# Performance work log

Hardware: AMD Instinct MI355X
Metric: run time of the kernel (lower is better)

Reference implementation:

```python
import jax, jax.numpy as jnp
import numpy as np

N = 50000        # nodes
E = 800000       # edges
IN, H1, H2 = 512, 256, 128
NEG_SLOPE = 0.2


def setup_inputs() -> dict:
    key = jax.random.key(0)
    k = jax.random.split(key, 6)
    X = jax.random.normal(k[0], (N, IN), jnp.float32)
    edge_index = jax.random.randint(k[1], (2, E), 0, N, dtype=jnp.int64)
    # GCNConv params: linear weight (no bias in lin) + additive bias
    W1 = jax.random.normal(k[2], (IN, H1), jnp.float32) / np.sqrt(IN).astype(np.float32)
    b1 = jnp.zeros((H1,), jnp.float32)
    W2 = jax.random.normal(k[3], (H1, H2), jnp.float32) / np.sqrt(H1).astype(np.float32)
    b2 = jnp.zeros((H2,), jnp.float32)
    return {"X": X, "edge_index": edge_index, "W1": W1, "b1": b1, "W2": W2, "b2": b2}


def gcn_conv(x, edge_index, W, b):
    """PyG GCNConv: X' = D^{-1/2} (A + I) D^{-1/2} (X W) + b."""
    src, dst = edge_index[0], edge_index[1]
    # degree with self-loops (unit edge weights)
    deg = jnp.zeros((N,), x.dtype).at[dst].add(jnp.asarray(1.0, x.dtype)) + 1.0
    dinv = jax.lax.rsqrt(deg)
    h = x @ W                                   # dense transform first (in >= out)
    coef = dinv[src] * dinv[dst]                # [E]
    msgs = h[src] * coef[:, None]               # [E, out]
    agg = jax.ops.segment_sum(msgs, dst, num_segments=N)
    agg = agg + (dinv * dinv)[:, None] * h      # self-loop contribution
    return agg + b


def reference(X, edge_index, W1, b1, W2, b2):
    Z = jax.nn.leaky_relu(gcn_conv(X, edge_index, W1, b1), NEG_SLOPE)
    Z = jax.nn.leaky_relu(gcn_conv(Z, edge_index, W2, b2), NEG_SLOPE)
    return Z
```

## Files before the change

### kernel.cpp

```cpp
#include <hip/hip_runtime.h>

constexpr int N_NODES = 50000;
constexpr int N_EDGES = 800000;
constexpr int F_IN  = 512;
constexpr int F_H1  = 256;
constexpr int F_H2  = 128;

typedef short  short8  __attribute__((ext_vector_type(8)));
typedef float  f32x4   __attribute__((ext_vector_type(4)));
typedef unsigned short us4 __attribute__((ext_vector_type(4)));

__device__ __forceinline__ unsigned short bf16_rn(float f) {
  unsigned int u = __float_as_uint(f);
  return (unsigned short)((u + 0x7FFFu + ((u >> 16) & 1u)) >> 16);
}
__device__ __forceinline__ float bf16_tof(unsigned short h) {
  return __uint_as_float(((unsigned int)h) << 16);
}


__global__ __launch_bounds__(256) void k_count(const int* __restrict__ dst,
                                               int* __restrict__ cnt, int e) {
  int i = blockIdx.x * 256 + threadIdx.x;
  if (i < e) atomicAdd(&cnt[dst[i]], 1);
}

__global__ __launch_bounds__(1024) void k_scan(const int* __restrict__ cnt,
                                               int* __restrict__ rowstart,
                                               int* __restrict__ cursor,
                                               float* __restrict__ dinv, int n) {
  __shared__ int wsum[16];
  __shared__ int carry_s;
  const int t = threadIdx.x;
  const int wid = t >> 6, lane = t & 63;
  if (t == 0) { carry_s = 0; rowstart[0] = 0; }
  __syncthreads();
  for (int base = 0; base < n; base += 4096) {
    const int i0 = base + t * 4;
    int v[4];
    if (i0 + 4 <= n) {
      const int4 v4 = *(const int4*)&cnt[i0];
      v[0] = v4.x; v[1] = v4.y; v[2] = v4.z; v[3] = v4.w;
    } else {
#pragma unroll
      for (int j = 0; j < 4; ++j) v[j] = (i0 + j < n) ? cnt[i0 + j] : 0;
    }
#pragma unroll
    for (int j = 0; j < 4; ++j)
      if (i0 + j < n) dinv[i0 + j] = rsqrtf((float)v[j] + 1.0f);
    const int tsum = v[0] + v[1] + v[2] + v[3];
    int x = tsum;
#pragma unroll
    for (int off = 1; off < 64; off <<= 1) {
      int y = __shfl_up(x, off);
      if (lane >= off) x += y;
    }
    if (lane == 63) wsum[wid] = x;
    __syncthreads();
    if (wid == 0) {
      int s = (lane < 16) ? wsum[lane] : 0;
#pragma unroll
      for (int off = 1; off < 16; off <<= 1) {
        int y = __shfl_up(s, off);
        if (lane >= off) s += y;
      }
      if (lane < 16) wsum[lane] = s;
    }
    __syncthreads();
    const int carry = carry_s;
    const int woff = (wid == 0) ? 0 : wsum[wid - 1];
    int run = carry + woff + x - tsum;
#pragma unroll
    for (int j = 0; j < 4; ++j) {
      if (i0 + j < n) {
        cursor[i0 + j] = run;
        run += v[j];
        rowstart[i0 + j + 1] = run;
      }
    }
    __syncthreads();
    if (t == 1023) carry_s = carry + woff + x;
    __syncthreads();
  }
}

__global__ __launch_bounds__(256) void k_fill(const int* __restrict__ src,
                                              const int* __restrict__ dst,
                                              int* __restrict__ cursor,
                                              const float* __restrict__ dinv,
                                              int2* __restrict__ csr, int e) {
  int i = blockIdx.x * 256 + threadIdx.x;
  if (i < e) {
    const int s = src[i], d = dst[i];
    int slot = atomicAdd(&cursor[d], 1);
    csr[slot] = make_int2(s, __float_as_int(dinv[s] * dinv[d]));
  }
}

__global__ __launch_bounds__(256) void k_wsplit2(const float* __restrict__ W1,
                                                 unsigned short* __restrict__ W1h,
                                                 unsigned short* __restrict__ W1l,
                                                 const float* __restrict__ W2,
                                                 unsigned short* __restrict__ W2h,
                                                 unsigned short* __restrict__ W2l) {
  constexpr int T1 = F_IN * F_H1;
  constexpr int T2 = F_H1 * F_H2;
  int id = blockIdx.x * 256 + threadIdx.x;
  if (id < T1) {
    int n = id / F_IN, k = id - n * F_IN;
    float f = W1[(size_t)k * F_H1 + n];
    unsigned short h = bf16_rn(f);
    W1h[id] = h;
    W1l[id] = bf16_rn(f - bf16_tof(h));
  } else if (id < T1 + T2) {
    int id2 = id - T1;
    int n = id2 / F_H1, k = id2 - n * F_H1;
    float f = W2[(size_t)k * F_H2 + n];
    unsigned short h = bf16_rn(f);
    W2h[id2] = h;
    W2l[id2] = bf16_rn(f - bf16_tof(h));
  }
}

template <bool A_IS_F32>
__global__ __launch_bounds__(256) void k_mm(const float* __restrict__ Af,
                                            const unsigned short* __restrict__ Ah,
                                            const unsigned short* __restrict__ Al,
                                            const unsigned short* __restrict__ Bth,
                                            const unsigned short* __restrict__ Btl,
                                            float* __restrict__ C,
                                            unsigned short* __restrict__ Cb,
                                            int M, int N, int K) {
  __shared__ unsigned short Ah_s[128 * 64];
  __shared__ unsigned short Al_s[128 * 64];
  __shared__ unsigned short Bh_s[128 * 64];
  __shared__ unsigned short Bl_s[128 * 64];
  const int tid = threadIdx.x;
  const int wid = tid >> 6, lane = tid & 63;
  const int wm = wid >> 1, wn = wid & 1;
  const int lr = lane & 15, lg = lane >> 4;
  const int row0 = blockIdx.x * 128, col0 = blockIdx.y * 128;

  f32x4 acc[4][4] = {};

  float4 af0[4], af1[4];
  short8 ahr[4], alr[4];
  short8 bhr[4], blr[4];

  const int r_ld = tid >> 3, g_ld = tid & 7;
  const bool arow_ok = (row0 + r_ld) < M;

  auto load_tile = [&](int k0) {
#pragma unroll
    for (int c = 0; c < 4; ++c) {
      const int r = c * 32 + r_ld;
      const int gr = row0 + r;
      if (A_IS_F32) {
        af0[c] = make_float4(0.f, 0.f, 0.f, 0.f);
        af1[c] = af0[c];
        if (gr < M) {
          const float* ap = Af + (size_t)gr * K + k0 + g_ld * 8;
          af0[c] = *(const float4*)ap;
          af1[c] = *(const float4*)(ap + 4);
        }
      } else {
        ahr[c] = short8{};
        alr[c] = short8{};
        if (gr < M) {
          ahr[c] = *(const short8*)&Ah[(size_t)gr * K + k0 + g_ld * 8];
          alr[c] = *(const short8*)&Al[(size_t)gr * K + k0 + g_ld * 8];
        }
      }
      const int gcol = col0 + r;
      bhr[c] = *(const short8*)&Bth[(size_t)gcol * K + k0 + g_ld * 8];
      blr[c] = *(const short8*)&Btl[(size_t)gcol * K + k0 + g_ld * 8];
    }
  };

  auto store_tile = [&]() {
#pragma unroll
    for (int c = 0; c < 4; ++c) {
      const int r = c * 32 + r_ld;
      const int gs = g_ld ^ (r & 7);
      const int doff = r * 64 + gs * 8;
      if (A_IS_F32) {
        const float fv[8] = {af0[c].x, af0[c].y, af0[c].z, af0[c].w,
                             af1[c].x, af1[c].y, af1[c].z, af1[c].w};
        unsigned short hv[8], lv[8];
#pragma unroll
        for (int j = 0; j < 8; ++j) {
          hv[j] = bf16_rn(fv[j]);
          lv[j] = bf16_rn(fv[j] - bf16_tof(hv[j]));
        }
        us4* dh = (us4*)&Ah_s[doff];
        us4* dl = (us4*)&Al_s[doff];
        dh[0] = us4{hv[0], hv[1], hv[2], hv[3]};
        dh[1] = us4{hv[4], hv[5], hv[6], hv[7]};
        dl[0] = us4{lv[0], lv[1], lv[2], lv[3]};
        dl[1] = us4{lv[4], lv[5], lv[6], lv[7]};
      } else {
        *(short8*)&Ah_s[doff] = ahr[c];
        *(short8*)&Al_s[doff] = alr[c];
      }
      *(short8*)&Bh_s[doff] = bhr[c];
      *(short8*)&Bl_s[doff] = blr[c];
    }
  };

  const int nsteps = K >> 6;
  load_tile(0);
  for (int s = 0; s < nsteps; ++s) {
    store_tile();
    __syncthreads();
    if (s + 1 < nsteps) load_tile((s + 1) << 6);
#pragma unroll
    for (int kk = 0; kk < 2; ++kk) {
      short8 ah[4], al[4], bh[4], bl[4];
#pragma unroll
      for (int m = 0; m < 4; ++m) {
        const int r = wm * 64 + m * 16 + lr;
        const int g = kk * 4 + lg;
        const int off = r * 64 + (g ^ (r & 7)) * 8;
        ah[m] = *(const short8*)&Ah_s[off];
        al[m] = *(const short8*)&Al_s[off];
      }
#pragma unroll
      for (int n = 0; n < 4; ++n) {
        const int r = wn * 64 + n * 16 + lr;
        const int g = kk * 4 + lg;
        const int off = r * 64 + (g ^ (r & 7)) * 8;
        bh[n] = *(const short8*)&Bh_s[off];
        bl[n] = *(const short8*)&Bl_s[off];
      }
#pragma unroll
      for (int m = 0; m < 4; ++m)
#pragma unroll
        for (int n = 0; n < 4; ++n)
          acc[m][n] = __builtin_amdgcn_mfma_f32_16x16x32_bf16(ah[m], bh[n],
                                                              acc[m][n], 0, 0, 0);
#pragma unroll
      for (int m = 0; m < 4; ++m)
#pragma unroll
        for (int n = 0; n < 4; ++n) {
          acc[m][n] = __builtin_amdgcn_mfma_f32_16x16x32_bf16(ah[m], bl[n],
                                                              acc[m][n], 0, 0, 0);
          acc[m][n] = __builtin_amdgcn_mfma_f32_16x16x32_bf16(al[m], bh[n],
                                                              acc[m][n], 0, 0, 0);
        }
    }
    __syncthreads();
  }
#pragma unroll
  for (int m = 0; m < 4; ++m) {
#pragma unroll
    for (int j = 0; j < 4; ++j) {
      const int row = row0 + wm * 64 + m * 16 + (lane >> 4) * 4 + j;
      if (row < M) {
        const size_t boff = (size_t)row * N + col0 + wn * 64 + (lane & 15);
        float* cp = C + boff;
#pragma unroll
        for (int n = 0; n < 4; ++n) cp[n * 16] = acc[m][n][j];
        if (Cb) {
          unsigned short* cbp = Cb + boff;
#pragma unroll
          for (int n = 0; n < 4; ++n) cbp[n * 16] = bf16_rn(acc[m][n][j]);
        }
      }
    }
  }
}

template <int F, bool SPLIT_OUT, bool BF16G>
__global__ __launch_bounds__(256) void k_agg(const float* __restrict__ hf,
                                             const unsigned short* __restrict__ hb,
                                             const int* __restrict__ rowstart,
                                             const int2* __restrict__ csr,
                                             const float* __restrict__ dinv,
                                             const float* __restrict__ bias,
                                             float* __restrict__ outp,
                                             unsigned short* __restrict__ outh,
                                             unsigned short* __restrict__ outl,
                                             int n) {
  constexpr int V = F / 64;
  const int node = (blockIdx.x * 256 + threadIdx.x) >> 6;
  const int lane = threadIdx.x & 63;
  if (node >= n) return;
  const float dn = dinv[node];
  const int e0 = rowstart[node];
  const int cnt = rowstart[node + 1] - e0;
  const int2* cp = csr + e0;
  float acc[V] = {};
  int i = 0;

  auto gather = [&](int s, float f[V]) {
    if constexpr (BF16G) {
      if constexpr (V == 4) {
        const uint2 u = *(const uint2*)(hb + (size_t)s * F + lane * 4);
        f[0] = __uint_as_float(u.x << 16);
        f[1] = __uint_as_float(u.x & 0xffff0000u);
        f[2] = __uint_as_float(u.y << 16);
        f[3] = __uint_as_float(u.y & 0xffff0000u);
      } else {
        const unsigned int u = *(const unsigned int*)(hb + (size_t)s * F + lane * 2);
        f[0] = __uint_as_float(u << 16);
        f[1] = __uint_as_float(u & 0xffff0000u);
      }
    } else {
      if constexpr (V == 4) {
        const float4 v = *(const float4*)(hf + (size_t)s * F + lane * 4);
        f[0] = v.x; f[1] = v.y; f[2] = v.z; f[3] = v.w;
      } else {
        const float2 v = *(const float2*)(hf + (size_t)s * F + lane * 2);
        f[0] = v.x; f[1] = v.y;
      }
    }
  };

  for (; i + 4 <= cnt; i += 4) {
    const int2 p0 = cp[i], p1 = cp[i + 1], p2 = cp[i + 2], p3 = cp[i + 3];
    float f0[V], f1[V], f2[V], f3[V];
    gather(p0.x, f0);
    gather(p1.x, f1);
    gather(p2.x, f2);
    gather(p3.x, f3);
    const float c0 = __int_as_float(p0.y), c1 = __int_as_float(p1.y);
    const float c2 = __int_as_float(p2.y), c3 = __int_as_float(p3.y);
#pragma unroll
    for (int j = 0; j < V; ++j)
      acc[j] += c0 * f0[j] + c1 * f1[j] + c2 * f2[j] + c3 * f3[j];
  }
  for (; i < cnt; ++i) {
    const int2 p = cp[i];
    const float c = __int_as_float(p.y);
    float f[V];
    gather(p.x, f);
#pragma unroll
    for (int j = 0; j < V; ++j) acc[j] += c * f[j];
  }

  const float sc = dn * dn;
  const float* hp = hf + (size_t)node * F + lane * V;
  const float* bp = bias + lane * V;
  float r[V];
#pragma unroll
  for (int j = 0; j < V; ++j) {
    float t = acc[j] + sc * hp[j] + bp[j];
    r[j] = fmaxf(t, 0.2f * t);
  }
  if constexpr (SPLIT_OUT) {
    unsigned short hh[V], ll[V];
#pragma unroll
    for (int j = 0; j < V; ++j) {
      hh[j] = bf16_rn(r[j]);
      ll[j] = bf16_rn(r[j] - bf16_tof(hh[j]));
    }
    if constexpr (V == 4) {
      *(us4*)&outh[(size_t)node * F + lane * 4] = us4{hh[0], hh[1], hh[2], hh[3]};
      *(us4*)&outl[(size_t)node * F + lane * 4] = us4{ll[0], ll[1], ll[2], ll[3]};
    } else {
#pragma unroll
      for (int j = 0; j < V; ++j) {
        outh[(size_t)node * F + lane * V + j] = hh[j];
        outl[(size_t)node * F + lane * V + j] = ll[j];
      }
    }
  } else {
    float* op = outp + (size_t)node * F + lane * V;
    if constexpr (V == 4) {
      *(float4*)op = make_float4(r[0], r[1], r[2], r[3]);
    } else {
      *(float2*)op = make_float2(r[0], r[1]);
    }
  }
}

extern "C" void kernel_launch(void* const* d_in, const int* in_sizes, int n_in,
                              void* d_out, int out_size, void* d_ws, size_t ws_size,
                              hipStream_t stream) {
  const float* X  = (const float*)d_in[0];
  const int*   ei = (const int*)d_in[1];
  const float* W1 = (const float*)d_in[2];
  const float* b1 = (const float*)d_in[3];
  const float* W2 = (const float*)d_in[4];
  const float* b2 = (const float*)d_in[5];
  float* out = (float*)d_out;
  const int* src = ei;
  const int* dst = ei + N_EDGES;

  char* p0 = (char*)d_ws;
  char* p = p0;
  float* h1 = (float*)p;                    p += (size_t)N_NODES * F_H1 * 4;
  unsigned short* z1h = (unsigned short*)p; p += (size_t)N_NODES * F_H1 * 2;
  unsigned short* z1l = (unsigned short*)p; p += (size_t)N_NODES * F_H1 * 2;
  unsigned short* Wt1h = (unsigned short*)p; p += (size_t)F_IN * F_H1 * 2;
  unsigned short* Wt1l = (unsigned short*)p; p += (size_t)F_IN * F_H1 * 2;
  unsigned short* Wt2h = (unsigned short*)p; p += (size_t)F_H1 * F_H2 * 2;
  unsigned short* Wt2l = (unsigned short*)p; p += (size_t)F_H1 * F_H2 * 2;
  float* dinv = (float*)p;                  p += 50048 * 4;
  int* counts = (int*)p;                    p += 50048 * 4;
  int* rowstart = (int*)p;                  p += 50056 * 4;
  int* cursor = (int*)p;                    p += 50048 * 4;
  int2* csr = (int2*)p;                     p += (size_t)N_EDGES * 8;
  unsigned short* h1b = (unsigned short*)p; p += (size_t)N_NODES * F_H1 * 2;
  unsigned short* h2b = h1b;
  float* h2 = h1;
  const bool GB = (size_t)(p - p0) <= ws_size;

  hipMemsetAsync(counts, 0, N_NODES * sizeof(int), stream);
  k_count<<<(N_EDGES + 255) / 256, 256, 0, stream>>>(dst, counts, N_EDGES);
  k_scan<<<1, 1024, 0, stream>>>(counts, rowstart, cursor, dinv, N_NODES);
  k_fill<<<(N_EDGES + 255) / 256, 256, 0, stream>>>(src, dst, cursor, dinv, csr,
                                                    N_EDGES);

  k_wsplit2<<<(F_IN * F_H1 + F_H1 * F_H2 + 255) / 256, 256, 0, stream>>>(
      W1, Wt1h, Wt1l, W2, Wt2h, Wt2l);

  dim3 g1((N_NODES + 127) / 128, F_H1 / 128);
  k_mm<true><<<g1, 256, 0, stream>>>(X, nullptr, nullptr, Wt1h, Wt1l, h1,
                                     GB ? h1b : nullptr, N_NODES, F_H1, F_IN);
  if (GB)
    k_agg<F_H1, true, true><<<(N_NODES + 3) / 4, 256, 0, stream>>>(
        h1, h1b, rowstart, csr, dinv, b1, nullptr, z1h, z1l, N_NODES);
  else
    k_agg<F_H1, true, false><<<(N_NODES + 3) / 4, 256, 0, stream>>>(
        h1, nullptr, rowstart, csr, dinv, b1, nullptr, z1h, z1l, N_NODES);

  dim3 g2((N_NODES + 127) / 128, F_H2 / 128);
  k_mm<false><<<g2, 256, 0, stream>>>(nullptr, z1h, z1l, Wt2h, Wt2l, h2,
                                      GB ? h2b : nullptr, N_NODES, F_H2, F_H1);
  if (GB)
    k_agg<F_H2, false, true><<<(N_NODES + 3) / 4, 256, 0, stream>>>(
        h2, h2b, rowstart, csr, dinv, b2, out, nullptr, nullptr, N_NODES);
  else
    k_agg<F_H2, false, false><<<(N_NODES + 3) / 4, 256, 0, stream>>>(
        h2, nullptr, rowstart, csr, dinv, b2, out, nullptr, nullptr, N_NODES);
}
```

Baseline: 348.8 us.

## Store GEMM output as bf16 hi/lo pairs and use 8-wave GEMM blocks

The GEMM now writes its result as a bf16 high/low split instead of fp32 plus an optional bf16 copy. Aggregation gathers only the high half and rebuilds the self-loop term from hi+lo, which removes the fp32 intermediate and the workspace-size fallback path. The GEMM block grows from 256 to 512 threads, with each wave covering a 64x32 tile instead of 64x64, to raise occupancy. The cost is that the self term is now rounded to about 16 mantissa bits, and each wave reuses its shared-memory A fragments across fewer columns.

```diff
diff --git a/kernel.cpp b/kernel.cpp
--- a/kernel.cpp
+++ b/kernel.cpp
@@ -123,37 +123,36 @@
 }
 
 template <bool A_IS_F32>
-__global__ __launch_bounds__(256) void k_mm(const float* __restrict__ Af,
-                                            const unsigned short* __restrict__ Ah,
-                                            const unsigned short* __restrict__ Al,
-                                            const unsigned short* __restrict__ Bth,
-                                            const unsigned short* __restrict__ Btl,
-                                            float* __restrict__ C,
-                                            unsigned short* __restrict__ Cb,
-                                            int M, int N, int K) {
+__global__ __launch_bounds__(512, 4) void k_mm(const float* __restrict__ Af,
+                                               const unsigned short* __restrict__ Ah,
+                                               const unsigned short* __restrict__ Al,
+                                               const unsigned short* __restrict__ Bth,
+                                               const unsigned short* __restrict__ Btl,
+                                               unsigned short* __restrict__ Chh,
+                                               unsigned short* __restrict__ Cll,
+                                               int M, int N, int K) {
   __shared__ unsigned short Ah_s[128 * 64];
   __shared__ unsigned short Al_s[128 * 64];
   __shared__ unsigned short Bh_s[128 * 64];
   __shared__ unsigned short Bl_s[128 * 64];
   const int tid = threadIdx.x;
   const int wid = tid >> 6, lane = tid & 63;
-  const int wm = wid >> 1, wn = wid & 1;
+  const int wm = wid >> 2, wn = wid & 3;
   const int lr = lane & 15, lg = lane >> 4;
   const int row0 = blockIdx.x * 128, col0 = blockIdx.y * 128;
 
-  f32x4 acc[4][4] = {};
-
-  float4 af0[4], af1[4];
-  short8 ahr[4], alr[4];
-  short8 bhr[4], blr[4];
-
-  const int r_ld = tid >> 3, g_ld = tid & 7;
-  const bool arow_ok = (row0 + r_ld) < M;
+  f32x4 acc[4][2] = {};
+
+  float4 af0[2], af1[2];
+  short8 ahr[2], alr[2];
+  short8 bhr[2], blr[2];
+
+  const int r_base = tid >> 3, g_ld = tid & 7;
 
   auto load_tile = [&](int k0) {
 #pragma unroll
-    for (int c = 0; c < 4; ++c) {
-      const int r = c * 32 + r_ld;
+    for (int c = 0; c < 2; ++c) {
+      const int r = c * 64 + r_base;
       const int gr = row0 + r;
       if (A_IS_F32) {
         af0[c] = make_float4(0.f, 0.f, 0.f, 0.f);
@@ -179,8 +178,8 @@
 
   auto store_tile = [&]() {
 #pragma unroll
-    for (int c = 0; c < 4; ++c) {
-      const int r = c * 32 + r_ld;
+    for (int c = 0; c < 2; ++c) {
+      const int r = c * 64 + r_base;
       const int gs = g_ld ^ (r & 7);
       const int doff = r * 64 + gs * 8;
       if (A_IS_F32) {
@@ -215,7 +214,7 @@
     if (s + 1 < nsteps) load_tile((s + 1) << 6);
 #pragma unroll
     for (int kk = 0; kk < 2; ++kk) {
-      short8 ah[4], al[4], bh[4], bl[4];
+      short8 ah[4], al[4], bh[2], bl[2];
 #pragma unroll
       for (int m = 0; m < 4; ++m) {
         const int r = wm * 64 + m * 16 + lr;
@@ -225,8 +224,8 @@
         al[m] = *(const short8*)&Al_s[off];
       }
 #pragma unroll
-      for (int n = 0; n < 4; ++n) {
-        const int r = wn * 64 + n * 16 + lr;
+      for (int n = 0; n < 2; ++n) {
+        const int r = wn * 32 + n * 16 + lr;
         const int g = kk * 4 + lg;
         const int off = r * 64 + (g ^ (r & 7)) * 8;
         bh[n] = *(const short8*)&Bh_s[off];
@@ -235,13 +234,13 @@
 #pragma unroll
       for (int m = 0; m < 4; ++m)
 #pragma unroll
-        for (int n = 0; n < 4; ++n)
+        for (int n = 0; n < 2; ++n)
           acc[m][n] = __builtin_amdgcn_mfma_f32_16x16x32_bf16(ah[m], bh[n],
                                                               acc[m][n], 0, 0, 0);
 #pragma unroll
       for (int m = 0; m < 4; ++m)
 #pragma unroll
-        for (int n = 0; n < 4; ++n) {
+        for (int n = 0; n < 2; ++n) {
           acc[m][n] = __builtin_amdgcn_mfma_f32_16x16x32_bf16(ah[m], bl[n],
                                                               acc[m][n], 0, 0, 0);
           acc[m][n] = __builtin_amdgcn_mfma_f32_16x16x32_bf16(al[m], bh[n],
@@ -256,23 +255,22 @@
     for (int j = 0; j < 4; ++j) {
       const int row = row0 + wm * 64 + m * 16 + (lane >> 4) * 4 + j;
       if (row < M) {
-        const size_t boff = (size_t)row * N + col0 + wn * 64 + (lane & 15);
-        float* cp = C + boff;
-#pragma unroll
-        for (int n = 0; n < 4; ++n) cp[n * 16] = acc[m][n][j];
-        if (Cb) {
-          unsigned short* cbp = Cb + boff;
-#pragma unroll
-          for (int n = 0; n < 4; ++n) cbp[n * 16] = bf16_rn(acc[m][n][j]);
+        const size_t base = (size_t)row * N + col0 + wn * 32 + lr;
+#pragma unroll
+        for (int n = 0; n < 2; ++n) {
+          const float v = acc[m][n][j];
+          const unsigned short hv = bf16_rn(v);
+          Chh[base + n * 16] = hv;
+          Cll[base + n * 16] = bf16_rn(v - bf16_tof(hv));
         }
       }
     }
   }
 }
 
-template <int F, bool SPLIT_OUT, bool BF16G>
-__global__ __launch_bounds__(256) void k_agg(const float* __restrict__ hf,
-                                             const unsigned short* __restrict__ hb,
+template <int F, bool SPLIT_OUT>
+__global__ __launch_bounds__(256) void k_agg(const unsigned short* __restrict__ hh,
+                                             const unsigned short* __restrict__ hl,
                                              const int* __restrict__ rowstart,
                                              const int2* __restrict__ csr,
                                              const float* __restrict__ dinv,
@@ -293,26 +291,16 @@
   int i = 0;
 
   auto gather = [&](int s, float f[V]) {
-    if constexpr (BF16G) {
-      if constexpr (V == 4) {
-        const uint2 u = *(const uint2*)(hb + (size_t)s * F + lane * 4);
-        f[0] = __uint_as_float(u.x << 16);
-        f[1] = __uint_as_float(u.x & 0xffff0000u);
-        f[2] = __uint_as_float(u.y << 16);
-        f[3] = __uint_as_float(u.y & 0xffff0000u);
-      } else {
-        const unsigned int u = *(const unsigned int*)(hb + (size_t)s * F + lane * 2);
-        f[0] = __uint_as_float(u << 16);
-        f[1] = __uint_as_float(u & 0xffff0000u);
-      }
+    if constexpr (V == 4) {
+      const uint2 u = *(const uint2*)(hh + (size_t)s * F + lane * 4);
+      f[0] = __uint_as_float(u.x << 16);
+      f[1] = __uint_as_float(u.x & 0xffff0000u);
+      f[2] = __uint_as_float(u.y << 16);
+      f[3] = __uint_as_float(u.y & 0xffff0000u);
     } else {
-      if constexpr (V == 4) {
-        const float4 v = *(const float4*)(hf + (size_t)s * F + lane * 4);
-        f[0] = v.x; f[1] = v.y; f[2] = v.z; f[3] = v.w;
-      } else {
-        const float2 v = *(const float2*)(hf + (size_t)s * F + lane * 2);
-        f[0] = v.x; f[1] = v.y;
-      }
+      const unsigned int u = *(const unsigned int*)(hh + (size_t)s * F + lane * 2);
+      f[0] = __uint_as_float(u << 16);
+      f[1] = __uint_as_float(u & 0xffff0000u);
     }
   };
 
@@ -339,29 +327,31 @@
   }
 
   const float sc = dn * dn;
-  const float* hp = hf + (size_t)node * F + lane * V;
+  const unsigned short* shp = hh + (size_t)node * F + lane * V;
+  const unsigned short* slp = hl + (size_t)node * F + lane * V;
   const float* bp = bias + lane * V;
   float r[V];
 #pragma unroll
   for (int j = 0; j < V; ++j) {
-    float t = acc[j] + sc * hp[j] + bp[j];
+    const float hself = bf16_tof(shp[j]) + bf16_tof(slp[j]);
+    float t = acc[j] + sc * hself + bp[j];
     r[j] = fmaxf(t, 0.2f * t);
   }
   if constexpr (SPLIT_OUT) {
-    unsigned short hh[V], ll[V];
+    unsigned short hv[V], lv[V];
 #pragma unroll
     for (int j = 0; j < V; ++j) {
-      hh[j] = bf16_rn(r[j]);
-      ll[j] = bf16_rn(r[j] - bf16_tof(hh[j]));
+      hv[j] = bf16_rn(r[j]);
+      lv[j] = bf16_rn(r[j] - bf16_tof(hv[j]));
     }
     if constexpr (V == 4) {
-      *(us4*)&outh[(size_t)node * F + lane * 4] = us4{hh[0], hh[1], hh[2], hh[3]};
-      *(us4*)&outl[(size_t)node * F + lane * 4] = us4{ll[0], ll[1], ll[2], ll[3]};
+      *(us4*)&outh[(size_t)node * F + lane * 4] = us4{hv[0], hv[1], hv[2], hv[3]};
+      *(us4*)&outl[(size_t)node * F + lane * 4] = us4{lv[0], lv[1], lv[2], lv[3]};
     } else {
 #pragma unroll
       for (int j = 0; j < V; ++j) {
-        outh[(size_t)node * F + lane * V + j] = hh[j];
-        outl[(size_t)node * F + lane * V + j] = ll[j];
+        outh[(size_t)node * F + lane * V + j] = hv[j];
+        outl[(size_t)node * F + lane * V + j] = lv[j];
       }
     }
   } else {
@@ -387,9 +377,9 @@
   const int* src = ei;
   const int* dst = ei + N_EDGES;
 
-  char* p0 = (char*)d_ws;
-  char* p = p0;
-  float* h1 = (float*)p;                    p += (size_t)N_NODES * F_H1 * 4;
+  char* p = (char*)d_ws;
+  unsigned short* h1h = (unsigned short*)p; p += (size_t)N_NODES * F_H1 * 2;
+  unsigned short* h1l = (unsigned short*)p; p += (size_t)N_NODES * F_H1 * 2;
   unsigned short* z1h = (unsigned short*)p; p += (size_t)N_NODES * F_H1 * 2;
   unsigned short* z1l = (unsigned short*)p; p += (size_t)N_NODES * F_H1 * 2;
   unsigned short* Wt1h = (unsigned short*)p; p += (size_t)F_IN * F_H1 * 2;
@@ -401,10 +391,8 @@
   int* rowstart = (int*)p;                  p += 50056 * 4;
   int* cursor = (int*)p;                    p += 50048 * 4;
   int2* csr = (int2*)p;                     p += (size_t)N_EDGES * 8;
-  unsigned short* h1b = (unsigned short*)p; p += (size_t)N_NODES * F_H1 * 2;
-  unsigned short* h2b = h1b;
-  float* h2 = h1;
-  const bool GB = (size_t)(p - p0) <= ws_size;
+  unsigned short* h2h = h1h;
+  unsigned short* h2l = h1l;
 
   hipMemsetAsync(counts, 0, N_NODES * sizeof(int), stream);
   k_count<<<(N_EDGES + 255) / 256, 256, 0, stream>>>(dst, counts, N_EDGES);
@@ -416,22 +404,14 @@
       W1, Wt1h, Wt1l, W2, Wt2h, Wt2l);
 
   dim3 g1((N_NODES + 127) / 128, F_H1 / 128);
-  k_mm<true><<<g1, 256, 0, stream>>>(X, nullptr, nullptr, Wt1h, Wt1l, h1,
-                                     GB ? h1b : nullptr, N_NODES, F_H1, F_IN);
-  if (GB)
-    k_agg<F_H1, true, true><<<(N_NODES + 3) / 4, 256, 0, stream>>>(
-        h1, h1b, rowstart, csr, dinv, b1, nullptr, z1h, z1l, N_NODES);
-  else
-    k_agg<F_H1, true, false><<<(N_NODES + 3) / 4, 256, 0, stream>>>(
-        h1, nullptr, rowstart, csr, dinv, b1, nullptr, z1h, z1l, N_NODES);
+  k_mm<true><<<g1, 512, 0, stream>>>(X, nullptr, nullptr, Wt1h, Wt1l, h1h, h1l,
+                                     N_NODES, F_H1, F_IN);
+  k_agg<F_H1, true><<<(N_NODES + 3) / 4, 256, 0, stream>>>(
+      h1h, h1l, rowstart, csr, dinv, b1, nullptr, z1h, z1l, N_NODES);
 
   dim3 g2((N_NODES + 127) / 128, F_H2 / 128);
-  k_mm<false><<<g2, 256, 0, stream>>>(nullptr, z1h, z1l, Wt2h, Wt2l, h2,
-                                      GB ? h2b : nullptr, N_NODES, F_H2, F_H1);
-  if (GB)
-    k_agg<F_H2, false, true><<<(N_NODES + 3) / 4, 256, 0, stream>>>(
-        h2, h2b, rowstart, csr, dinv, b2, out, nullptr, nullptr, N_NODES);
-  else
-    k_agg<F_H2, false, false><<<(N_NODES + 3) / 4, 256, 0, stream>>>(
-        h2, nullptr, rowstart, csr, dinv, b2, out, nullptr, nullptr, N_NODES);
-}
+  k_mm<false><<<g2, 512, 0, stream>>>(nullptr, z1h, z1l, Wt2h, Wt2l, h2h, h2l,
+                                      N_NODES, F_H2, F_H1);
+  k_agg<F_H2, false><<<(N_NODES + 3) / 4, 256, 0, stream>>>(
+      h2h, h2l, rowstart, csr, dinv, b2, out, nullptr, nullptr, N_NODES);
+}
```

Result: faster. 332.9 us (-4.6%).
